# Optimization experiments

Hardware: AMD Instinct MI355X
Metric: run time of the kernel (lower is better)

Reference implementation:

```python
import jax, jax.numpy as jnp
import numpy as np

BATCH = 8192
NUM_CLASSES = 10000
FEAT_DIM = 256


def setup_inputs() -> dict:
    key = jax.random.key(0)
    k1, k2, k3 = jax.random.split(key, 3)
    x = jax.random.normal(k1, (BATCH, FEAT_DIM), dtype=jnp.float32)
    labels = jax.random.randint(k2, (BATCH,), 0, NUM_CLASSES, dtype=jnp.int64)
    centers = jax.random.normal(k3, (NUM_CLASSES, FEAT_DIM), dtype=jnp.float32)
    return {"x": x, "labels": labels, "centers": centers}


def reference(x, labels, centers):
    batch_size = x.shape[0]
    num_classes = centers.shape[0]
    # distmat[b,c] = ||x_b||^2 + ||center_c||^2 - 2 <x_b, center_c>   [B, C]
    x_sq = jnp.sum(x * x, axis=1, keepdims=True)            # [B, 1]
    c_sq = jnp.sum(centers * centers, axis=1)[None, :]      # [1, C]
    distmat = x_sq + c_sq - 2.0 * jnp.einsum('bd,cd->bc', x, centers)
    # mask: one-hot of labels over classes
    mask = (labels[:, None] == jnp.arange(num_classes)[None, :]).astype(distmat.dtype)
    dist = distmat * mask
    # torch clamps ALL entries (masked zeros become 1e-12) before summing
    loss = jnp.sum(jnp.clip(dist, 1e-12, 1e12)) / batch_size
    return loss
```

## Files before the change

### kernel.cpp

```cpp
#include <hip/hip_runtime.h>


#define NBLOCKS 256
#define TPB 256
#define WAVES_PER_BLOCK (TPB / 64)

__global__ __launch_bounds__(TPB) void centerloss_partial(
    const float* __restrict__ x,
    const int* __restrict__ labels,
    const float* __restrict__ centers,
    float* __restrict__ partial,
    int B)
{
    const int lane   = threadIdx.x & 63;
    const int wave   = (blockIdx.x * TPB + threadIdx.x) >> 6;
    const int nwaves = (gridDim.x * TPB) >> 6;

    float acc = 0.0f;
    for (int b = wave; b < B; b += nwaves) {
        const int lbl = labels[b];
        const float4 xv = ((const float4*)(x       + (size_t)b   * 256))[lane];
        const float4 cv = ((const float4*)(centers + (size_t)lbl * 256))[lane];

        float v = xv.x * xv.x + xv.y * xv.y + xv.z * xv.z + xv.w * xv.w;
        v += cv.x * cv.x + cv.y * cv.y + cv.z * cv.z + cv.w * cv.w;
        v -= 2.0f * (xv.x * cv.x + xv.y * cv.y + xv.z * cv.z + xv.w * cv.w);

        #pragma unroll
        for (int off = 32; off > 0; off >>= 1)
            v += __shfl_down(v, off, 64);

        if (lane == 0)
            acc += fminf(fmaxf(v, 1e-12f), 1e12f);
    }

    __shared__ float s[WAVES_PER_BLOCK];
    if (lane == 0) s[threadIdx.x >> 6] = acc;
    __syncthreads();
    if (threadIdx.x == 0) {
        float t = 0.0f;
        #pragma unroll
        for (int i = 0; i < WAVES_PER_BLOCK; ++i) t += s[i];
        partial[blockIdx.x] = t;
    }
}

__global__ __launch_bounds__(NBLOCKS) void centerloss_final(
    const float* __restrict__ partial,
    float* __restrict__ out,
    int B, int C)
{
    float v = partial[threadIdx.x];
    #pragma unroll
    for (int off = 32; off > 0; off >>= 1)
        v += __shfl_down(v, off, 64);

    __shared__ float s[NBLOCKS / 64];
    if ((threadIdx.x & 63) == 0) s[threadIdx.x >> 6] = v;
    __syncthreads();
    if (threadIdx.x == 0) {
        float t = 0.0f;
        #pragma unroll
        for (int i = 0; i < NBLOCKS / 64; ++i) t += s[i];
        double loss = (double)t / (double)B + (double)(C - 1) * 1e-12;
        out[0] = (float)loss;
    }
}

extern "C" void kernel_launch(void* const* d_in, const int* in_sizes, int n_in,
                              void* d_out, int out_size, void* d_ws, size_t ws_size,
                              hipStream_t stream)
{
    const float* x       = (const float*)d_in[0];
    const int*   labels  = (const int*)d_in[1];
    const float* centers = (const float*)d_in[2];

    const int B = in_sizes[1];
    const int D = in_sizes[0] / B;
    const int C = in_sizes[2] / D;
    (void)D;

    float* partial = (float*)d_ws;
    float* out     = (float*)d_out;

    centerloss_partial<<<NBLOCKS, TPB, 0, stream>>>(x, labels, centers, partial, B);
    centerloss_final<<<1, NBLOCKS, 0, stream>>>(partial, out, B, C);
}
```

Baseline: 73.71 us.

## Assign one wave per row with a full grid and reduce per-row partials

Replaces the grid-stride loop over 256 blocks with a launch of one wave per batch row (1024 blocks of 512 threads). Each wave writes its clamped row distance to the workspace, and a 1024-thread final kernel sums all B values. The aim is to expose more memory-level parallelism for the gathered center rows and the x reads, at the cost of a larger workspace write and a longer serial reduction in the single final block.

```diff
diff --git a/kernel.cpp b/kernel.cpp
--- a/kernel.cpp
+++ b/kernel.cpp
@@ -1,67 +1,56 @@
 #include <hip/hip_runtime.h>
 
 
-#define NBLOCKS 256
-#define TPB 256
-#define WAVES_PER_BLOCK (TPB / 64)
+#define TPB1 512
+#define TPB2 1024
 
-__global__ __launch_bounds__(TPB) void centerloss_partial(
+__global__ __launch_bounds__(TPB1) void centerloss_partial(
     const float* __restrict__ x,
     const int* __restrict__ labels,
     const float* __restrict__ centers,
     float* __restrict__ partial,
     int B)
 {
-    const int lane   = threadIdx.x & 63;
-    const int wave   = (blockIdx.x * TPB + threadIdx.x) >> 6;
-    const int nwaves = (gridDim.x * TPB) >> 6;
+    const int lane = threadIdx.x & 63;
+    const int b    = (blockIdx.x * TPB1 + threadIdx.x) >> 6;
+    if (b >= B) return;
 
-    float acc = 0.0f;
-    for (int b = wave; b < B; b += nwaves) {
-        const int lbl = labels[b];
-        const float4 xv = ((const float4*)(x       + (size_t)b   * 256))[lane];
-        const float4 cv = ((const float4*)(centers + (size_t)lbl * 256))[lane];
+    const int lbl = labels[b];
+    const float4 xv = ((const float4*)(x       + (size_t)b   * 256))[lane];
+    const float4 cv = ((const float4*)(centers + (size_t)lbl * 256))[lane];
 
-        float v = xv.x * xv.x + xv.y * xv.y + xv.z * xv.z + xv.w * xv.w;
-        v += cv.x * cv.x + cv.y * cv.y + cv.z * cv.z + cv.w * cv.w;
-        v -= 2.0f * (xv.x * cv.x + xv.y * cv.y + xv.z * cv.z + xv.w * cv.w);
+    float v = xv.x * xv.x + xv.y * xv.y + xv.z * xv.z + xv.w * xv.w;
+    v += cv.x * cv.x + cv.y * cv.y + cv.z * cv.z + cv.w * cv.w;
+    v -= 2.0f * (xv.x * cv.x + xv.y * cv.y + xv.z * cv.z + xv.w * cv.w);
 
-        #pragma unroll
-        for (int off = 32; off > 0; off >>= 1)
-            v += __shfl_down(v, off, 64);
-
-        if (lane == 0)
-            acc += fminf(fmaxf(v, 1e-12f), 1e12f);
-    }
-
-    __shared__ float s[WAVES_PER_BLOCK];
-    if (lane == 0) s[threadIdx.x >> 6] = acc;
-    __syncthreads();
-    if (threadIdx.x == 0) {
-        float t = 0.0f;
-        #pragma unroll
-        for (int i = 0; i < WAVES_PER_BLOCK; ++i) t += s[i];
-        partial[blockIdx.x] = t;
-    }
-}
-
-__global__ __launch_bounds__(NBLOCKS) void centerloss_final(
-    const float* __restrict__ partial,
-    float* __restrict__ out,
-    int B, int C)
-{
-    float v = partial[threadIdx.x];
     #pragma unroll
     for (int off = 32; off > 0; off >>= 1)
         v += __shfl_down(v, off, 64);
 
-    __shared__ float s[NBLOCKS / 64];
+    if (lane == 0)
+        partial[b] = fminf(fmaxf(v, 1e-12f), 1e12f);
+}
+
+__global__ __launch_bounds__(TPB2) void centerloss_final(
+    const float* __restrict__ partial,
+    float* __restrict__ out,
+    int n, int B, int C)
+{
+    float v = 0.0f;
+    for (int i = threadIdx.x; i < n; i += TPB2)
+        v += partial[i];
+
+    #pragma unroll
+    for (int off = 32; off > 0; off >>= 1)
+        v += __shfl_down(v, off, 64);
+
+    __shared__ float s[TPB2 / 64];
     if ((threadIdx.x & 63) == 0) s[threadIdx.x >> 6] = v;
     __syncthreads();
     if (threadIdx.x == 0) {
         float t = 0.0f;
         #pragma unroll
-        for (int i = 0; i < NBLOCKS / 64; ++i) t += s[i];
+        for (int i = 0; i < TPB2 / 64; ++i) t += s[i];
         double loss = (double)t / (double)B + (double)(C - 1) * 1e-12;
         out[0] = (float)loss;
     }
@@ -78,11 +67,11 @@
     const int B = in_sizes[1];
     const int D = in_sizes[0] / B;
     const int C = in_sizes[2] / D;
-    (void)D;
 
     float* partial = (float*)d_ws;
     float* out     = (float*)d_out;
 
-    centerloss_partial<<<NBLOCKS, TPB, 0, stream>>>(x, labels, centers, partial, B);
-    centerloss_final<<<1, NBLOCKS, 0, stream>>>(partial, out, B, C);
+    const int nblocks = (B * 64 + TPB1 - 1) / TPB1;
+    centerloss_partial<<<nblocks, TPB1, 0, stream>>>(x, labels, centers, partial, B);
+    centerloss_final<<<1, TPB2, 0, stream>>>(partial, out, B, B, C);
 }
```

Measured after the change: 69.23 us. 1.06x faster.
